# Performance work log

Measured on AMD Instinct MI355X. Metric: run time of the kernel, lower is better.

The kernel has to match this reference:

```python
import jax, jax.numpy as jnp
import numpy as np

def setup_inputs() -> dict:
    key = jax.random.key(0)
    k1, k2 = jax.random.split(key)
    B, S, D, R = 16, 1024, 1024, 128
    batch = jax.random.normal(k1, (B, S, D), dtype=jnp.float32)
    # probe parameter initialized uniform(-0.05, 0.05) as in the torch module
    proj = jax.random.uniform(k2, (D, R), dtype=jnp.float32, minval=-0.05, maxval=0.05)
    return {"batch": batch, "proj": proj}

def reference(batch, proj):
    # transformed: [B, S, R]
    t = jnp.matmul(batch, proj)
    # squared L2 distances for all pairs: ||t_i||^2 + ||t_j||^2 - 2 t_i . t_j
    sq_norms = jnp.sum(t * t, axis=-1)                      # [B, S]
    cross = jnp.einsum('bir,bjr->bij', t, t)                # [B, S, S]
    d = sq_norms[:, :, None] + sq_norms[:, None, :] - 2.0 * cross
    return jnp.maximum(d, 0.0)  # clamp tiny negative values from the identity
```

## Files before the change

kernel.cpp:

```cpp
#include <hip/hip_runtime.h>

typedef __attribute__((ext_vector_type(8))) __bf16 bf16x8;
typedef __attribute__((ext_vector_type(4))) __bf16 bf16x4;
typedef __attribute__((ext_vector_type(4))) float f32x4;

#define B_ 16
#define S_ 1024
#define D_ 1024
#define R_ 128

__global__ __launch_bounds__(256) void k_transpose(const float* __restrict__ proj,
                                                   __bf16* __restrict__ projT) {
    __shared__ __bf16 tile[64][66];
    const int k0 = blockIdx.x * 64;
    const int r0 = blockIdx.y * 64;
#pragma unroll
    for (int it = 0; it < 16; ++it) {
        int idx = it * 256 + threadIdx.x;
        int kk = idx >> 6, rr = idx & 63;
        tile[kk][rr] = (__bf16)proj[(size_t)(k0 + kk) * R_ + (r0 + rr)];
    }
    __syncthreads();
#pragma unroll
    for (int it = 0; it < 16; ++it) {
        int idx = it * 256 + threadIdx.x;
        int rr = idx >> 6, kk = idx & 63;
        projT[(size_t)(r0 + rr) * D_ + (k0 + kk)] = tile[kk][rr];
    }
}

#define STG_LD 264
__global__ __launch_bounds__(256, 4) void k_proj(const float* __restrict__ batch,
                                                 const __bf16* __restrict__ projT,
                                                 __bf16* __restrict__ t,
                                                 float* __restrict__ sqn) {
    const int wave = threadIdx.x >> 6;
    const int lane = threadIdx.x & 63;
    const int ln = lane & 15;
    const int q  = lane >> 4;
    const int m0 = blockIdx.x * 16;
    const int kbase = wave * 256;

    __shared__ __align__(16) char smraw[4 * 16 * STG_LD * 2];
    __bf16 (*stg)[STG_LD] =
        reinterpret_cast<__bf16(*)[STG_LD]>(smraw + wave * (16 * STG_LD * 2));

    const float* abase = batch + (size_t)m0 * D_ + kbase;
#pragma unroll
    for (int r = 0; r < 16; ++r) {
        float4 v = *(const float4*)(abase + (size_t)r * D_ + lane * 4);
        bf16x4 h = {(__bf16)v.x, (__bf16)v.y, (__bf16)v.z, (__bf16)v.w};
        *(bf16x4*)&stg[r][lane * 4] = h;
    }

    f32x4 acc[8];
#pragma unroll
    for (int ni = 0; ni < 8; ++ni) acc[ni] = f32x4{0.f, 0.f, 0.f, 0.f};

    const __bf16* bbase = projT + kbase;
    const int ka0 = q * 8;
    bf16x8 bcur[8], bnxt[8];
#pragma unroll
    for (int ni = 0; ni < 8; ++ni)
        bcur[ni] = *(const bf16x8*)(bbase + (size_t)(ni * 16 + ln) * D_ + ka0);

#pragma unroll
    for (int k0 = 0; k0 < 8; ++k0) {
        if (k0 < 7) {
            const int kan = ka0 + (k0 + 1) * 32;
#pragma unroll
            for (int ni = 0; ni < 8; ++ni)
                bnxt[ni] = *(const bf16x8*)(bbase + (size_t)(ni * 16 + ln) * D_ + kan);
        }
        bf16x8 af = *(const bf16x8*)&stg[ln][k0 * 32 + ka0];
#pragma unroll
        for (int ni = 0; ni < 8; ++ni)
            acc[ni] = __builtin_amdgcn_mfma_f32_16x16x32_bf16(af, bcur[ni], acc[ni], 0, 0, 0);
        if (k0 < 7) {
#pragma unroll
            for (int ni = 0; ni < 8; ++ni) bcur[ni] = bnxt[ni];
        }
    }

    __syncthreads();
    f32x4 (*red)[64] = reinterpret_cast<f32x4(*)[64]>(smraw);
    float (*sqpart)[16] = reinterpret_cast<float(*)[16]>(smraw + 32768);
#pragma unroll
    for (int ni = 0; ni < 8; ++ni) red[wave * 8 + ni][lane] = acc[ni];
    __syncthreads();

    float sq[4] = {0.f, 0.f, 0.f, 0.f};
#pragma unroll
    for (int p = 0; p < 2; ++p) {
        const int ni = wave * 2 + p;
        f32x4 v = red[ni][lane];
#pragma unroll
        for (int w = 1; w < 4; ++w) {
            f32x4 u = red[w * 8 + ni][lane];
            v[0] += u[0]; v[1] += u[1]; v[2] += u[2]; v[3] += u[3];
        }
#pragma unroll
        for (int r = 0; r < 4; ++r) {
            __bf16 h = (__bf16)v[r];
            t[(size_t)(m0 + q * 4 + r) * R_ + ni * 16 + ln] = h;
            float f = (float)h;
            sq[r] += f * f;
        }
    }
#pragma unroll
    for (int r = 0; r < 4; ++r) {
#pragma unroll
        for (int off = 1; off < 16; off <<= 1)
            sq[r] += __shfl_xor(sq[r], off, 64);
    }
    if (ln == 0) {
#pragma unroll
        for (int r = 0; r < 4; ++r) sqpart[wave][q * 4 + r] = sq[r];
    }
    __syncthreads();
    if (threadIdx.x < 16) {
        float s = sqpart[0][threadIdx.x] + sqpart[1][threadIdx.x] +
                  sqpart[2][threadIdx.x] + sqpart[3][threadIdx.x];
        sqn[m0 + threadIdx.x] = s;
    }
}

#define GLP 264
__global__ __launch_bounds__(256, 2) void k_gram(const __bf16* __restrict__ t,
                                                 const float* __restrict__ sqn,
                                                 float* __restrict__ out) {
    const int b = blockIdx.z;
    const int wave = threadIdx.x >> 6;
    const int lane = threadIdx.x & 63;
    const int ln = lane & 15;
    const int q  = lane >> 4;
    const int wi = wave >> 1, wj = wave & 1;
    const int i0b = blockIdx.y * 128;
    const int j0b = blockIdx.x * 128;
    const __bf16* tb = t + (size_t)b * S_ * R_;
    const float* sqb = sqn + (size_t)b * S_;

    __shared__ __align__(16) char sm[256 * GLP];
    {
        const __bf16* tis = tb + (size_t)i0b * R_;
        const __bf16* tjs = tb + (size_t)j0b * R_;
#pragma unroll
        for (int it = 0; it < 16; ++it) {
            int u = it * 256 + threadIdx.x;
            int row = u >> 4, ch = u & 15;
            const __bf16* src = (row < 128) ? (tis + (size_t)row * R_)
                                            : (tjs + (size_t)(row - 128) * R_);
            float4 v = *(const float4*)(src + ch * 8);
            *(float4*)(sm + (size_t)row * GLP + ch * 16) = v;
        }
    }
    __syncthreads();

    f32x4 acc[4][4];
#pragma unroll
    for (int mi = 0; mi < 4; ++mi)
#pragma unroll
        for (int ni = 0; ni < 4; ++ni) acc[mi][ni] = f32x4{0.f, 0.f, 0.f, 0.f};

    const char* ibase = sm + (size_t)(wi * 64) * GLP;
    const char* jbase = sm + (size_t)(128 + wj * 64) * GLP;
#pragma unroll
    for (int k0 = 0; k0 < R_; k0 += 32) {
        const int kab = (k0 + q * 8) * 2;
        bf16x8 af[4], bfm[4];
#pragma unroll
        for (int mi = 0; mi < 4; ++mi)
            af[mi] = *(const bf16x8*)(ibase + (size_t)(mi * 16 + ln) * GLP + kab);
#pragma unroll
        for (int ni = 0; ni < 4; ++ni)
            bfm[ni] = *(const bf16x8*)(jbase + (size_t)(ni * 16 + ln) * GLP + kab);
#pragma unroll
        for (int mi = 0; mi < 4; ++mi)
#pragma unroll
            for (int ni = 0; ni < 4; ++ni)
                acc[mi][ni] = __builtin_amdgcn_mfma_f32_16x16x32_bf16(
                    af[mi], bfm[ni], acc[mi][ni], 0, 0, 0);
    }

    const int i0 = i0b + wi * 64;
    const int j0 = j0b + wj * 64;
    float sqj[4];
#pragma unroll
    for (int ni = 0; ni < 4; ++ni) sqj[ni] = sqb[j0 + ni * 16 + ln];

    float* outb = out + (size_t)b * S_ * S_;
#pragma unroll
    for (int mi = 0; mi < 4; ++mi) {
        float4 si4 = *(const float4*)(sqb + i0 + mi * 16 + q * 4);
#pragma unroll
        for (int ni = 0; ni < 4; ++ni) {
            const int j = j0 + ni * 16 + ln;
            float4 o;
            o.x = fmaxf(si4.x + sqj[ni] - 2.f * acc[mi][ni][0], 0.f);
            o.y = fmaxf(si4.y + sqj[ni] - 2.f * acc[mi][ni][1], 0.f);
            o.z = fmaxf(si4.z + sqj[ni] - 2.f * acc[mi][ni][2], 0.f);
            o.w = fmaxf(si4.w + sqj[ni] - 2.f * acc[mi][ni][3], 0.f);
            *(float4*)(outb + (size_t)j * S_ + i0 + mi * 16 + q * 4) = o;
        }
    }
}

extern "C" void kernel_launch(void* const* d_in, const int* in_sizes, int n_in,
                              void* d_out, int out_size, void* d_ws, size_t ws_size,
                              hipStream_t stream) {
    const float* batch = (const float*)d_in[0];
    const float* proj  = (const float*)d_in[1];
    float* out = (float*)d_out;

    char* ws = (char*)d_ws;
    __bf16* t     = (__bf16*)ws;
    __bf16* projT = (__bf16*)(ws + (size_t)B_ * S_ * R_ * 2);
    float*  sqn   = (float*)(ws + (size_t)B_ * S_ * R_ * 2
                                + (size_t)R_ * D_ * 2);

    k_transpose<<<dim3(D_ / 64, R_ / 64), 256, 0, stream>>>(proj, projT);
    k_proj<<<dim3((B_ * S_) / 16), 256, 0, stream>>>(batch, projT, t, sqn);
    k_gram<<<dim3(S_ / 128, S_ / 128, B_), 256, 0, stream>>>(t, sqn, out);
}
```

Before: 159.6 us.

## Split-K projection GEMM with LDS-staged tiles, atomic accumulation and finalize pass

The projection kernel now gives each block a 64-row by 256-K slice. Both the batch tile and the projT tile are staged in shared memory, so the projection matrix is reused across four waves instead of being fetched per wave from global memory. Partial results are combined with float atomicAdd into a zeroed fp32 buffer, and a new finalize kernel converts that buffer to bf16 and computes the squared norms. This adds a memset, an extra kernel launch, roughly 8 MB of fp32 atomic traffic, and a dependence on workspace size. The old kernel is kept as a fallback for small workspaces.

```diff
diff --git a/kernel.cpp b/kernel.cpp
--- a/kernel.cpp
+++ b/kernel.cpp
@@ -29,100 +29,77 @@
     }
 }
 
-#define STG_LD 264
-__global__ __launch_bounds__(256, 4) void k_proj(const float* __restrict__ batch,
-                                                 const __bf16* __restrict__ projT,
-                                                 __bf16* __restrict__ t,
-                                                 float* __restrict__ sqn) {
-    const int wave = threadIdx.x >> 6;
-    const int lane = threadIdx.x & 63;
-    const int ln = lane & 15;
-    const int q  = lane >> 4;
-    const int m0 = blockIdx.x * 16;
-    const int kbase = wave * 256;
-
-    __shared__ __align__(16) char smraw[4 * 16 * STG_LD * 2];
-    __bf16 (*stg)[STG_LD] =
-        reinterpret_cast<__bf16(*)[STG_LD]>(smraw + wave * (16 * STG_LD * 2));
-
-    const float* abase = batch + (size_t)m0 * D_ + kbase;
-#pragma unroll
-    for (int r = 0; r < 16; ++r) {
-        float4 v = *(const float4*)(abase + (size_t)r * D_ + lane * 4);
+#define LDA 136
+__global__ __launch_bounds__(256, 3) void k_proj5(const float* __restrict__ batch,
+                                                  const __bf16* __restrict__ projT,
+                                                  float* __restrict__ tacc) {
+    __shared__ __align__(16) __bf16 smA[64 * LDA];
+    __shared__ __align__(16) __bf16 smB[128 * LDA];
+    const int t = threadIdx.x;
+    const int wave = t >> 6, lane = t & 63;
+    const int ln = lane & 15, q = lane >> 4;
+    const int m0 = blockIdx.x * 64;
+    const int kq0 = blockIdx.y * 256;
+
+    f32x4 acc[8];
+#pragma unroll
+    for (int ni = 0; ni < 8; ++ni) acc[ni] = f32x4{0.f, 0.f, 0.f, 0.f};
+
+    for (int c = 0; c < 2; ++c) {
+        const int kq = kq0 + c * 128;
+#pragma unroll
+        for (int i = 0; i < 8; ++i) {
+            int u = i * 256 + t;
+            int row = u >> 5, pos = u & 31;
+            float4 v = *(const float4*)(batch + (size_t)(m0 + row) * D_ + kq + pos * 4);
+            bf16x4 h = {(__bf16)v.x, (__bf16)v.y, (__bf16)v.z, (__bf16)v.w};
+            *(bf16x4*)&smA[row * LDA + pos * 4] = h;
+        }
+#pragma unroll
+        for (int i = 0; i < 8; ++i) {
+            int u = i * 256 + t;
+            int row = u >> 4, pos = u & 15;
+            bf16x8 v = *(const bf16x8*)(projT + (size_t)row * D_ + kq + pos * 8);
+            *(bf16x8*)&smB[row * LDA + pos * 8] = v;
+        }
+        __syncthreads();
+#pragma unroll
+        for (int k0 = 0; k0 < 4; ++k0) {
+            bf16x8 af = *(const bf16x8*)&smA[(wave * 16 + ln) * LDA + k0 * 32 + q * 8];
+#pragma unroll
+            for (int ni = 0; ni < 8; ++ni) {
+                bf16x8 bf = *(const bf16x8*)&smB[(ni * 16 + ln) * LDA + k0 * 32 + q * 8];
+                acc[ni] = __builtin_amdgcn_mfma_f32_16x16x32_bf16(af, bf, acc[ni], 0, 0, 0);
+            }
+        }
+        __syncthreads();
+    }
+    const int mrow = m0 + wave * 16 + q * 4;
+#pragma unroll
+    for (int ni = 0; ni < 8; ++ni)
+#pragma unroll
+        for (int r = 0; r < 4; ++r)
+            atomicAdd(&tacc[(size_t)(mrow + r) * R_ + ni * 16 + ln], acc[ni][r]);
+}
+
+__global__ __launch_bounds__(256) void k_finalize(const float* __restrict__ tacc,
+                                                  __bf16* __restrict__ t_,
+                                                  float* __restrict__ sqn) {
+    const int u = blockIdx.x * 256 + threadIdx.x;
+    const int base = u * 32;
+    const int row = u >> 2;
+    float sq = 0.f;
+#pragma unroll
+    for (int i = 0; i < 8; ++i) {
+        float4 v = *(const float4*)(tacc + base + i * 4);
         bf16x4 h = {(__bf16)v.x, (__bf16)v.y, (__bf16)v.z, (__bf16)v.w};
-        *(bf16x4*)&stg[r][lane * 4] = h;
-    }
-
-    f32x4 acc[8];
-#pragma unroll
-    for (int ni = 0; ni < 8; ++ni) acc[ni] = f32x4{0.f, 0.f, 0.f, 0.f};
-
-    const __bf16* bbase = projT + kbase;
-    const int ka0 = q * 8;
-    bf16x8 bcur[8], bnxt[8];
-#pragma unroll
-    for (int ni = 0; ni < 8; ++ni)
-        bcur[ni] = *(const bf16x8*)(bbase + (size_t)(ni * 16 + ln) * D_ + ka0);
-
-#pragma unroll
-    for (int k0 = 0; k0 < 8; ++k0) {
-        if (k0 < 7) {
-            const int kan = ka0 + (k0 + 1) * 32;
-#pragma unroll
-            for (int ni = 0; ni < 8; ++ni)
-                bnxt[ni] = *(const bf16x8*)(bbase + (size_t)(ni * 16 + ln) * D_ + kan);
-        }
-        bf16x8 af = *(const bf16x8*)&stg[ln][k0 * 32 + ka0];
-#pragma unroll
-        for (int ni = 0; ni < 8; ++ni)
-            acc[ni] = __builtin_amdgcn_mfma_f32_16x16x32_bf16(af, bcur[ni], acc[ni], 0, 0, 0);
-        if (k0 < 7) {
-#pragma unroll
-            for (int ni = 0; ni < 8; ++ni) bcur[ni] = bnxt[ni];
-        }
-    }
-
-    __syncthreads();
-    f32x4 (*red)[64] = reinterpret_cast<f32x4(*)[64]>(smraw);
-    float (*sqpart)[16] = reinterpret_cast<float(*)[16]>(smraw + 32768);
-#pragma unroll
-    for (int ni = 0; ni < 8; ++ni) red[wave * 8 + ni][lane] = acc[ni];
-    __syncthreads();
-
-    float sq[4] = {0.f, 0.f, 0.f, 0.f};
-#pragma unroll
-    for (int p = 0; p < 2; ++p) {
-        const int ni = wave * 2 + p;
-        f32x4 v = red[ni][lane];
-#pragma unroll
-        for (int w = 1; w < 4; ++w) {
-            f32x4 u = red[w * 8 + ni][lane];
-            v[0] += u[0]; v[1] += u[1]; v[2] += u[2]; v[3] += u[3];
-        }
-#pragma unroll
-        for (int r = 0; r < 4; ++r) {
-            __bf16 h = (__bf16)v[r];
-            t[(size_t)(m0 + q * 4 + r) * R_ + ni * 16 + ln] = h;
-            float f = (float)h;
-            sq[r] += f * f;
-        }
-    }
-#pragma unroll
-    for (int r = 0; r < 4; ++r) {
-#pragma unroll
-        for (int off = 1; off < 16; off <<= 1)
-            sq[r] += __shfl_xor(sq[r], off, 64);
-    }
-    if (ln == 0) {
-#pragma unroll
-        for (int r = 0; r < 4; ++r) sqpart[wave][q * 4 + r] = sq[r];
-    }
-    __syncthreads();
-    if (threadIdx.x < 16) {
-        float s = sqpart[0][threadIdx.x] + sqpart[1][threadIdx.x] +
-                  sqpart[2][threadIdx.x] + sqpart[3][threadIdx.x];
-        sqn[m0 + threadIdx.x] = s;
-    }
+        *(bf16x4*)(t_ + base + i * 4) = h;
+        float a = (float)h[0], b = (float)h[1], c = (float)h[2], d = (float)h[3];
+        sq += a * a + b * b + c * c + d * d;
+    }
+    sq += __shfl_xor(sq, 1, 64);
+    sq += __shfl_xor(sq, 2, 64);
+    if ((threadIdx.x & 3) == 0) sqn[row] = sq;
 }
 
 #define GLP 264
@@ -205,6 +182,83 @@
     }
 }
 
+#define STG_LD 264
+__global__ __launch_bounds__(256, 4) void k_proj_fb(const float* __restrict__ batch,
+                                                    const __bf16* __restrict__ projT,
+                                                    __bf16* __restrict__ t,
+                                                    float* __restrict__ sqn) {
+    const int wave = threadIdx.x >> 6;
+    const int lane = threadIdx.x & 63;
+    const int ln = lane & 15;
+    const int q  = lane >> 4;
+    const int m0 = blockIdx.x * 16;
+    const int kbase = wave * 256;
+
+    __shared__ __align__(16) char smraw[4 * 16 * STG_LD * 2];
+    __bf16 (*stg)[STG_LD] =
+        reinterpret_cast<__bf16(*)[STG_LD]>(smraw + wave * (16 * STG_LD * 2));
+    const float* abase = batch + (size_t)m0 * D_ + kbase;
+#pragma unroll
+    for (int r = 0; r < 16; ++r) {
+        float4 v = *(const float4*)(abase + (size_t)r * D_ + lane * 4);
+        bf16x4 h = {(__bf16)v.x, (__bf16)v.y, (__bf16)v.z, (__bf16)v.w};
+        *(bf16x4*)&stg[r][lane * 4] = h;
+    }
+    f32x4 acc[8];
+#pragma unroll
+    for (int ni = 0; ni < 8; ++ni) acc[ni] = f32x4{0.f, 0.f, 0.f, 0.f};
+#pragma unroll
+    for (int k0 = 0; k0 < 256; k0 += 32) {
+        const int ka = k0 + q * 8;
+        bf16x8 af = *(const bf16x8*)&stg[ln][ka];
+#pragma unroll
+        for (int ni = 0; ni < 8; ++ni) {
+            bf16x8 bf = *(const bf16x8*)(projT + (size_t)(ni * 16 + ln) * D_ + kbase + ka);
+            acc[ni] = __builtin_amdgcn_mfma_f32_16x16x32_bf16(af, bf, acc[ni], 0, 0, 0);
+        }
+    }
+    __syncthreads();
+    f32x4 (*red)[64] = reinterpret_cast<f32x4(*)[64]>(smraw);
+    float (*sqpart)[16] = reinterpret_cast<float(*)[16]>(smraw + 32768);
+#pragma unroll
+    for (int ni = 0; ni < 8; ++ni) red[wave * 8 + ni][lane] = acc[ni];
+    __syncthreads();
+    float sq[4] = {0.f, 0.f, 0.f, 0.f};
+#pragma unroll
+    for (int p = 0; p < 2; ++p) {
+        const int ni = wave * 2 + p;
+        f32x4 v = red[ni][lane];
+#pragma unroll
+        for (int w = 1; w < 4; ++w) {
+            f32x4 u = red[w * 8 + ni][lane];
+            v[0] += u[0]; v[1] += u[1]; v[2] += u[2]; v[3] += u[3];
+        }
+#pragma unroll
+        for (int r = 0; r < 4; ++r) {
+            __bf16 h = (__bf16)v[r];
+            t[(size_t)(m0 + q * 4 + r) * R_ + ni * 16 + ln] = h;
+            float f = (float)h;
+            sq[r] += f * f;
+        }
+    }
+#pragma unroll
+    for (int r = 0; r < 4; ++r) {
+#pragma unroll
+        for (int off = 1; off < 16; off <<= 1)
+            sq[r] += __shfl_xor(sq[r], off, 64);
+    }
+    if (ln == 0) {
+#pragma unroll
+        for (int r = 0; r < 4; ++r) sqpart[wave][q * 4 + r] = sq[r];
+    }
+    __syncthreads();
+    if (threadIdx.x < 16) {
+        float s = sqpart[0][threadIdx.x] + sqpart[1][threadIdx.x] +
+                  sqpart[2][threadIdx.x] + sqpart[3][threadIdx.x];
+        sqn[m0 + threadIdx.x] = s;
+    }
+}
+
 extern "C" void kernel_launch(void* const* d_in, const int* in_sizes, int n_in,
                               void* d_out, int out_size, void* d_ws, size_t ws_size,
                               hipStream_t stream) {
@@ -213,12 +267,27 @@
     float* out = (float*)d_out;
 
     char* ws = (char*)d_ws;
-    __bf16* t     = (__bf16*)ws;
-    __bf16* projT = (__bf16*)(ws + (size_t)B_ * S_ * R_ * 2);
-    float*  sqn   = (float*)(ws + (size_t)B_ * S_ * R_ * 2
-                                + (size_t)R_ * D_ * 2);
-
-    k_transpose<<<dim3(D_ / 64, R_ / 64), 256, 0, stream>>>(proj, projT);
-    k_proj<<<dim3((B_ * S_) / 16), 256, 0, stream>>>(batch, projT, t, sqn);
-    k_gram<<<dim3(S_ / 128, S_ / 128, B_), 256, 0, stream>>>(t, sqn, out);
-}
+    const size_t TACC_B  = (size_t)B_ * S_ * R_ * 4;
+    const size_t T_B     = (size_t)B_ * S_ * R_ * 2;
+    const size_t PROJT_B = (size_t)R_ * D_ * 2;
+    const size_t SQN_B   = (size_t)B_ * S_ * 4;
+
+    if (ws_size >= TACC_B + T_B + PROJT_B + SQN_B) {
+        float*  tacc  = (float*)ws;
+        __bf16* t     = (__bf16*)(ws + TACC_B);
+        __bf16* projT = (__bf16*)(ws + TACC_B + T_B);
+        float*  sqn   = (float*)(ws + TACC_B + T_B + PROJT_B);
+        hipMemsetAsync(tacc, 0, TACC_B, stream);
+        k_transpose<<<dim3(D_ / 64, R_ / 64), 256, 0, stream>>>(proj, projT);
+        k_proj5<<<dim3((B_ * S_) / 64, 4), 256, 0, stream>>>(batch, projT, tacc);
+        k_finalize<<<dim3((B_ * S_ * R_) / 32 / 256), 256, 0, stream>>>(tacc, t, sqn);
+        k_gram<<<dim3(S_ / 128, S_ / 128, B_), 256, 0, stream>>>(t, sqn, out);
+    } else {
+        __bf16* t     = (__bf16*)ws;
+        __bf16* projT = (__bf16*)(ws + T_B);
+        float*  sqn   = (float*)(ws + T_B + PROJT_B);
+        k_transpose<<<dim3(D_ / 64, R_ / 64), 256, 0, stream>>>(proj, projT);
+        k_proj_fb<<<dim3((B_ * S_) / 16), 256, 0, stream>>>(batch, projT, t, sqn);
+        k_gram<<<dim3(S_ / 128, S_ / 128, B_), 256, 0, stream>>>(t, sqn, out);
+    }
+}
```

Measured after the change: 161.4 us. Within noise of the previous version (+1.1%).

## Restructure projection kernel to stage A and B tiles in LDS across K chunks

Applied to the files above, without the earlier changes.

The projection kernel changes from a split-K scheme, where each wave covered a quarter of K, loaded B fragments straight from global memory, and reduced partial sums through LDS, to a loop over eight K chunks of 128. Each chunk cooperatively stages the A rows (converted to bf16) and the whole projT chunk in shared memory, and each wave computes 32 output columns. This removes the cross-wave reduction and the per-wave global B loads. In exchange it adds two barriers per chunk, gives each wave far fewer MFMAs between syncs, and still reloads the full 256KB projT per block from L2.

```diff
diff --git a/kernel.cpp b/kernel.cpp
--- a/kernel.cpp
+++ b/kernel.cpp
@@ -29,80 +29,64 @@
     }
 }
 
-#define STG_LD 264
-__global__ __launch_bounds__(256, 4) void k_proj(const float* __restrict__ batch,
-                                                 const __bf16* __restrict__ projT,
-                                                 __bf16* __restrict__ t,
-                                                 float* __restrict__ sqn) {
-    const int wave = threadIdx.x >> 6;
-    const int lane = threadIdx.x & 63;
-    const int ln = lane & 15;
-    const int q  = lane >> 4;
+#define LDA6 136
+__global__ __launch_bounds__(256, 4) void k_proj6(const float* __restrict__ batch,
+                                                  const __bf16* __restrict__ projT,
+                                                  __bf16* __restrict__ t_,
+                                                  float* __restrict__ sqn) {
+    __shared__ __align__(16) __bf16 smA[16 * LDA6];
+    __shared__ __align__(16) __bf16 smB[128 * LDA6];
+    __shared__ float sqpart[4][16];
+    const int t = threadIdx.x;
+    const int wave = t >> 6, lane = t & 63;
+    const int ln = lane & 15, q = lane >> 4;
     const int m0 = blockIdx.x * 16;
-    const int kbase = wave * 256;
-
-    __shared__ __align__(16) char smraw[4 * 16 * STG_LD * 2];
-    __bf16 (*stg)[STG_LD] =
-        reinterpret_cast<__bf16(*)[STG_LD]>(smraw + wave * (16 * STG_LD * 2));
-
-    const float* abase = batch + (size_t)m0 * D_ + kbase;
-#pragma unroll
-    for (int r = 0; r < 16; ++r) {
-        float4 v = *(const float4*)(abase + (size_t)r * D_ + lane * 4);
-        bf16x4 h = {(__bf16)v.x, (__bf16)v.y, (__bf16)v.z, (__bf16)v.w};
-        *(bf16x4*)&stg[r][lane * 4] = h;
-    }
-
-    f32x4 acc[8];
-#pragma unroll
-    for (int ni = 0; ni < 8; ++ni) acc[ni] = f32x4{0.f, 0.f, 0.f, 0.f};
-
-    const __bf16* bbase = projT + kbase;
-    const int ka0 = q * 8;
-    bf16x8 bcur[8], bnxt[8];
-#pragma unroll
-    for (int ni = 0; ni < 8; ++ni)
-        bcur[ni] = *(const bf16x8*)(bbase + (size_t)(ni * 16 + ln) * D_ + ka0);
-
-#pragma unroll
-    for (int k0 = 0; k0 < 8; ++k0) {
-        if (k0 < 7) {
-            const int kan = ka0 + (k0 + 1) * 32;
-#pragma unroll
-            for (int ni = 0; ni < 8; ++ni)
-                bnxt[ni] = *(const bf16x8*)(bbase + (size_t)(ni * 16 + ln) * D_ + kan);
-        }
-        bf16x8 af = *(const bf16x8*)&stg[ln][k0 * 32 + ka0];
-#pragma unroll
-        for (int ni = 0; ni < 8; ++ni)
-            acc[ni] = __builtin_amdgcn_mfma_f32_16x16x32_bf16(af, bcur[ni], acc[ni], 0, 0, 0);
-        if (k0 < 7) {
-#pragma unroll
-            for (int ni = 0; ni < 8; ++ni) bcur[ni] = bnxt[ni];
-        }
-    }
-
-    __syncthreads();
-    f32x4 (*red)[64] = reinterpret_cast<f32x4(*)[64]>(smraw);
-    float (*sqpart)[16] = reinterpret_cast<float(*)[16]>(smraw + 32768);
-#pragma unroll
-    for (int ni = 0; ni < 8; ++ni) red[wave * 8 + ni][lane] = acc[ni];
-    __syncthreads();
+
+    const int arow = t >> 4, aseg = t & 15;
+    const int brow = t >> 1, bhalf = t & 1;
+
+    f32x4 acc[2];
+    acc[0] = f32x4{0.f, 0.f, 0.f, 0.f};
+    acc[1] = f32x4{0.f, 0.f, 0.f, 0.f};
+
+    for (int c = 0; c < 8; ++c) {
+        const int kq = c * 128;
+        {
+            const float* src = batch + (size_t)(m0 + arow) * D_ + kq + aseg * 4;
+#pragma unroll
+            for (int p = 0; p < 2; ++p) {
+                float4 v = *(const float4*)(src + p * 64);
+                bf16x4 h = {(__bf16)v.x, (__bf16)v.y, (__bf16)v.z, (__bf16)v.w};
+                *(bf16x4*)&smA[arow * LDA6 + p * 64 + aseg * 4] = h;
+            }
+        }
+        {
+            const __bf16* src = projT + (size_t)brow * D_ + kq + bhalf * 64;
+            __bf16* dst = &smB[brow * LDA6 + bhalf * 64];
+#pragma unroll
+            for (int i = 0; i < 8; ++i)
+                *(bf16x8*)(dst + i * 8) = *(const bf16x8*)(src + i * 8);
+        }
+        __syncthreads();
+#pragma unroll
+        for (int k0 = 0; k0 < 4; ++k0) {
+            bf16x8 af = *(const bf16x8*)&smA[ln * LDA6 + k0 * 32 + q * 8];
+#pragma unroll
+            for (int ni = 0; ni < 2; ++ni) {
+                bf16x8 bf = *(const bf16x8*)&smB[(wave * 32 + ni * 16 + ln) * LDA6 + k0 * 32 + q * 8];
+                acc[ni] = __builtin_amdgcn_mfma_f32_16x16x32_bf16(af, bf, acc[ni], 0, 0, 0);
+            }
+        }
+        __syncthreads();
+    }
 
     float sq[4] = {0.f, 0.f, 0.f, 0.f};
 #pragma unroll
-    for (int p = 0; p < 2; ++p) {
-        const int ni = wave * 2 + p;
-        f32x4 v = red[ni][lane];
-#pragma unroll
-        for (int w = 1; w < 4; ++w) {
-            f32x4 u = red[w * 8 + ni][lane];
-            v[0] += u[0]; v[1] += u[1]; v[2] += u[2]; v[3] += u[3];
-        }
+    for (int ni = 0; ni < 2; ++ni) {
 #pragma unroll
         for (int r = 0; r < 4; ++r) {
-            __bf16 h = (__bf16)v[r];
-            t[(size_t)(m0 + q * 4 + r) * R_ + ni * 16 + ln] = h;
+            __bf16 h = (__bf16)acc[ni][r];
+            t_[(size_t)(m0 + q * 4 + r) * R_ + wave * 32 + ni * 16 + ln] = h;
             float f = (float)h;
             sq[r] += f * f;
         }
@@ -118,10 +102,9 @@
         for (int r = 0; r < 4; ++r) sqpart[wave][q * 4 + r] = sq[r];
     }
     __syncthreads();
-    if (threadIdx.x < 16) {
-        float s = sqpart[0][threadIdx.x] + sqpart[1][threadIdx.x] +
-                  sqpart[2][threadIdx.x] + sqpart[3][threadIdx.x];
-        sqn[m0 + threadIdx.x] = s;
+    if (t < 16) {
+        float s = sqpart[0][t] + sqpart[1][t] + sqpart[2][t] + sqpart[3][t];
+        sqn[m0 + t] = s;
     }
 }
 
@@ -213,12 +196,14 @@
     float* out = (float*)d_out;
 
     char* ws = (char*)d_ws;
+    const size_t T_B     = (size_t)B_ * S_ * R_ * 2;
+    const size_t PROJT_B = (size_t)R_ * D_ * 2;
+
     __bf16* t     = (__bf16*)ws;
-    __bf16* projT = (__bf16*)(ws + (size_t)B_ * S_ * R_ * 2);
-    float*  sqn   = (float*)(ws + (size_t)B_ * S_ * R_ * 2
-                                + (size_t)R_ * D_ * 2);
+    __bf16* projT = (__bf16*)(ws + T_B);
+    float*  sqn   = (float*)(ws + T_B + PROJT_B);
 
     k_transpose<<<dim3(D_ / 64, R_ / 64), 256, 0, stream>>>(proj, projT);
-    k_proj<<<dim3((B_ * S_) / 16), 256, 0, stream>>>(batch, projT, t, sqn);
+    k_proj6<<<dim3((B_ * S_) / 16), 256, 0, stream>>>(batch, projT, t, sqn);
     k_gram<<<dim3(S_ / 128, S_ / 128, B_), 256, 0, stream>>>(t, sqn, out);
 }
```

Result: slower. 167.0 us (+4.6%).
